# Kernel tuning notes

Measured on AMD Instinct MI355X. Metric: run time of the kernel, lower is better.

## Reference

```python
import jax, jax.numpy as jnp
import numpy as np

NEG_SLOPE = 0.2


def gat_conv(x, src, dst, W, a_src, a_dst, b, concat):
    # x: [N, Fin]; W: [H*C, Fin]; a_src/a_dst: [H, C]; b: [H*C] or [C]
    N = x.shape[0]
    H, C = a_src.shape
    h = (x @ W.T).reshape(N, H, C)                      # per-head transform
    s_n = jnp.sum(h * a_src, axis=-1)                   # [N, H]
    d_n = jnp.sum(h * a_dst, axis=-1)                   # [N, H]
    e = jax.nn.leaky_relu(s_n[src] + d_n[dst], NEG_SLOPE)  # [E, H]
    # segment softmax over incoming edges of each destination node
    m = jax.ops.segment_max(e, dst, num_segments=N)
    m = jnp.where(jnp.isfinite(m), m, 0.0)
    ex = jnp.exp(e - m[dst])
    denom = jax.ops.segment_sum(ex, dst, num_segments=N)
    alpha = ex / (denom[dst] + 1e-16)                    # [E, H]
    msg = h[src] * alpha[:, :, None]                     # [E, H, C]
    out = jax.ops.segment_sum(msg, dst, num_segments=N)  # [N, H, C]
    out = out.reshape(N, H * C) if concat else out.mean(axis=1)
    return out + b


def setup_inputs() -> dict:
    key = jax.random.key(0)
    ks = jax.random.split(key, 16)
    N, E, F, C, H = 50000, 800000, 256, 128, 4
    sc = lambda fan_in: 1.0 / np.sqrt(fan_in)
    inp = {
        "x": jax.random.normal(ks[0], (N, F), dtype=jnp.float32),
        "edge_index": jax.random.randint(ks[1], (2, E), 0, N, dtype=jnp.int64),
        # layer 1: F -> H*C (concat)
        "W1": jax.random.normal(ks[2], (H * C, F), jnp.float32) * sc(F),
        "a_src1": jax.random.normal(ks[3], (H, C), jnp.float32) * sc(C),
        "a_dst1": jax.random.normal(ks[4], (H, C), jnp.float32) * sc(C),
        "b1": jnp.zeros((H * C,), jnp.float32),
        # layer 2: H*C -> H*C (concat)
        "W2": jax.random.normal(ks[5], (H * C, H * C), jnp.float32) * sc(H * C),
        "a_src2": jax.random.normal(ks[6], (H, C), jnp.float32) * sc(C),
        "a_dst2": jax.random.normal(ks[7], (H, C), jnp.float32) * sc(C),
        "b2": jnp.zeros((H * C,), jnp.float32),
        # layer 3: H*C -> C (heads=1, concat=False)
        "W3": jax.random.normal(ks[8], (C, H * C), jnp.float32) * sc(H * C),
        "a_src3": jax.random.normal(ks[9], (1, C), jnp.float32) * sc(C),
        "a_dst3": jax.random.normal(ks[10], (1, C), jnp.float32) * sc(C),
        "b3": jnp.zeros((C,), jnp.float32),
        # allocation head: C -> C//2 -> 1
        "Wh1": jax.random.normal(ks[11], (C // 2, C), jnp.float32) * sc(C),
        "bh1": jnp.zeros((C // 2,), jnp.float32),
        "Wh2": jax.random.normal(ks[12], (1, C // 2), jnp.float32) * sc(C // 2),
        "bh2": jnp.zeros((1,), jnp.float32),
    }
    return inp


def reference(x, edge_index, W1, a_src1, a_dst1, b1, W2, a_src2, a_dst2, b2,
              W3, a_src3, a_dst3, b3, Wh1, bh1, Wh2, bh2):
    N = x.shape[0]
    loops = jnp.arange(N, dtype=edge_index.dtype)
    src = jnp.concatenate([edge_index[0], loops])  # self-loops (PyG default)
    dst = jnp.concatenate([edge_index[1], loops])

    h = gat_conv(x, src, dst, W1, a_src1, a_dst1, b1, concat=True)
    h = jax.nn.elu(h)  # dropout is identity at inference
    h = gat_conv(h, src, dst, W2, a_src2, a_dst2, b2, concat=True)
    h = jax.nn.elu(h)
    embeddings = gat_conv(h, src, dst, W3, a_src3, a_dst3, b3, concat=False)

    z = jax.nn.relu(embeddings @ Wh1.T + bh1)
    allocation_scores = jax.nn.sigmoid(z @ Wh2.T + bh2)
    return embeddings, allocation_scores
```

## Files before the change

kernel.cpp:

```cpp
#include <hip/hip_runtime.h>
#include <math.h>

typedef _Float16 f16;
typedef f16 f16x2 __attribute__((ext_vector_type(2)));
typedef f16 f16x8 __attribute__((ext_vector_type(8)));
typedef float f32x4 __attribute__((ext_vector_type(4)));

template <int V> struct VecT;
template <> struct VecT<2> { using T = f16 __attribute__((ext_vector_type(2))); };
template <> struct VecT<8> { using T = f16 __attribute__((ext_vector_type(8))); };

__device__ __forceinline__ unsigned ordf(float f) {
  unsigned u = __float_as_uint(f);
  return (u >> 31) ? ~u : (u | 0x80000000u);
}
__device__ __forceinline__ float unordf(unsigned u) {
  return (u >> 31) ? __uint_as_float(u & 0x7fffffffu) : __uint_as_float(~u);
}


__global__ void k_count(const int* __restrict__ dstArr, int* __restrict__ cnt,
                        int E, int Et) {
  int i = blockIdx.x * blockDim.x + threadIdx.x;
  if (i >= Et) return;
  int d = (i < E) ? dstArr[i] : (i - E);
  atomicAdd(&cnt[d], 1);
}

__global__ __launch_bounds__(256) void k_scanA(const int* __restrict__ cnt,
                                               int* __restrict__ row_ptr,
                                               int* __restrict__ bsum, int n) {
  __shared__ int part[256];
  int t = threadIdx.x;
  int base = blockIdx.x * 1024 + t * 4;
  int4 v = make_int4(0, 0, 0, 0);
  if (base + 3 < n) v = *(const int4*)&cnt[base];
  else {
    if (base + 0 < n) v.x = cnt[base + 0];
    if (base + 1 < n) v.y = cnt[base + 1];
    if (base + 2 < n) v.z = cnt[base + 2];
    if (base + 3 < n) v.w = cnt[base + 3];
  }
  int s = v.x + v.y + v.z + v.w;
  part[t] = s;
  __syncthreads();
  for (int off = 1; off < 256; off <<= 1) {
    int x = (t >= off) ? part[t - off] : 0;
    __syncthreads();
    part[t] += x;
    __syncthreads();
  }
  int p0 = (t == 0) ? 0 : part[t - 1];
  int p1 = p0 + v.x, p2 = p1 + v.y, p3 = p2 + v.z;
  if (base + 0 < n) row_ptr[base + 0] = p0;
  if (base + 1 < n) row_ptr[base + 1] = p1;
  if (base + 2 < n) row_ptr[base + 2] = p2;
  if (base + 3 < n) row_ptr[base + 3] = p3;
  if (t == 255) bsum[blockIdx.x] = part[255];
}

__global__ __launch_bounds__(1024) void k_scanB(int* __restrict__ bsum, int nb) {
  __shared__ int part[1024];
  int t = threadIdx.x;
  int v = (t < nb) ? bsum[t] : 0;
  part[t] = v;
  __syncthreads();
  for (int off = 1; off < 1024; off <<= 1) {
    int x = (t >= off) ? part[t - off] : 0;
    __syncthreads();
    part[t] += x;
    __syncthreads();
  }
  if (t < nb) bsum[t] = (t == 0) ? 0 : part[t - 1];
  if (t == 1023) bsum[nb] = part[1023];
}

__global__ void k_scanC(int* __restrict__ row_ptr, int* __restrict__ cursor,
                        const int* __restrict__ bsum, int n, int nb) {
  int i = blockIdx.x * blockDim.x + threadIdx.x;
  if (i < n) {
    int v = row_ptr[i] + bsum[i >> 10];
    row_ptr[i] = v;
    cursor[i] = v;
  }
  if (i == n) row_ptr[n] = bsum[nb];
}

__global__ void k_fill(const int* __restrict__ dstArr, int* __restrict__ cursor,
                       int* __restrict__ perm, int E, int Et) {
  int i = blockIdx.x * blockDim.x + threadIdx.x;
  if (i >= Et) return;
  int d = (i < E) ? dstArr[i] : (i - E);
  int pos = atomicAdd(&cursor[d], 1);
  perm[pos] = i;
}

__global__ void k_f2h4(const float* s0, f16* d0, int n0,
                       const float* s1, f16* d1, int n1,
                       const float* s2, f16* d2, int n2,
                       const float* s3, f16* d3, int n3) {
  int i = blockIdx.x * blockDim.x + threadIdx.x;
  const float* s; f16* d;
  if (i < n0) { s = s0; d = d0; }
  else if ((i -= n0) < n1) { s = s1; d = d1; }
  else if ((i -= n1) < n2) { s = s2; d = d2; }
  else if ((i -= n2) < n3) { s = s3; d = d3; }
  else return;
  float4 v = ((const float4*)s)[i];
  union { f16 h[4]; double dd; } u;
  u.h[0] = (f16)v.x; u.h[1] = (f16)v.y; u.h[2] = (f16)v.z; u.h[3] = (f16)v.w;
  ((double*)d)[i] = u.dd;
}

__global__ __launch_bounds__(256) void k_hgemm_nt(
    const f16* __restrict__ A, const f16* __restrict__ B,
    f16* __restrict__ C, int M, int Nn, int K,
    const float* __restrict__ a_src, const float* __restrict__ a_dst,
    float* __restrict__ sArr, float* __restrict__ dArr,
    unsigned* __restrict__ gmaxU, int H) {
  __shared__ f16 As[128 * 32];
  __shared__ f16 Bs[128 * 32];
  int tid = threadIdx.x;
  int wave = tid >> 6, lane = tid & 63;
  int quad = lane >> 4, l16 = lane & 15;
  int m0 = blockIdx.y * 128, n0 = blockIdx.x * 128;
  int wm = (wave & 1) * 64, wn = (wave >> 1) * 64;

  int lr = lane >> 2;
  int lc = lane & 3;
  int chunk = lc ^ ((lr >> 1) & 3);
  int rb0 = wave * 16;
  int rb1 = 64 + wave * 16;
  int ga0 = m0 + rb0 + lr; if (ga0 >= M) ga0 = M - 1;
  int ga1 = m0 + rb1 + lr; if (ga1 >= M) ga1 = M - 1;
  const f16* gA0 = A + (size_t)ga0 * K + chunk * 8;
  const f16* gA1 = A + (size_t)ga1 * K + chunk * 8;
  const f16* gB0 = B + (size_t)(n0 + rb0 + lr) * K + chunk * 8;
  const f16* gB1 = B + (size_t)(n0 + rb1 + lr) * K + chunk * 8;
  f16* lA0 = &As[rb0 * 32];
  f16* lA1 = &As[rb1 * 32];
  f16* lB0 = &Bs[rb0 * 32];
  f16* lB1 = &Bs[rb1 * 32];

  int rsw = (quad ^ ((l16 >> 1) & 3)) * 8;
  const f16* Ard[4];
  const f16* Brd[4];
#pragma unroll
  for (int i = 0; i < 4; ++i) {
    Ard[i] = &As[(wm + i * 16 + l16) * 32 + rsw];
    Brd[i] = &Bs[(wn + i * 16 + l16) * 32 + rsw];
  }

  f32x4 acc[4][4];
#pragma unroll
  for (int i = 0; i < 4; ++i)
#pragma unroll
    for (int j = 0; j < 4; ++j) acc[i][j] = (f32x4)(0.f);

  for (int k0 = 0; k0 < K; k0 += 32) {
    __syncthreads();
    __builtin_amdgcn_global_load_lds(
        (const __attribute__((address_space(1))) void*)(gA0 + k0),
        (__attribute__((address_space(3))) void*)lA0, 16, 0, 0);
    __builtin_amdgcn_global_load_lds(
        (const __attribute__((address_space(1))) void*)(gA1 + k0),
        (__attribute__((address_space(3))) void*)lA1, 16, 0, 0);
    __builtin_amdgcn_global_load_lds(
        (const __attribute__((address_space(1))) void*)(gB0 + k0),
        (__attribute__((address_space(3))) void*)lB0, 16, 0, 0);
    __builtin_amdgcn_global_load_lds(
        (const __attribute__((address_space(1))) void*)(gB1 + k0),
        (__attribute__((address_space(3))) void*)lB1, 16, 0, 0);
    __syncthreads();
    f16x8 af[4], bf[4];
#pragma unroll
    for (int i = 0; i < 4; ++i) af[i] = *(const f16x8*)Ard[i];
#pragma unroll
    for (int j = 0; j < 4; ++j) bf[j] = *(const f16x8*)Brd[j];
#pragma unroll
    for (int i = 0; i < 4; ++i)
#pragma unroll
      for (int j = 0; j < 4; ++j)
        acc[i][j] = __builtin_amdgcn_mfma_f32_16x16x32_f16(af[i], bf[j], acc[i][j], 0, 0, 0);
  }

#pragma unroll
  for (int i = 0; i < 4; ++i) {
#pragma unroll
    for (int r = 0; r < 4; ++r) {
      int m = m0 + wm + i * 16 + quad * 4 + r;
      if (m < M) {
        f16* Cp = C + (size_t)m * Nn + n0 + wn + l16;
#pragma unroll
        for (int j = 0; j < 4; ++j) Cp[j * 16] = (f16)acc[i][j][r];
      }
    }
  }

  float av[4], ad[4];
#pragma unroll
  for (int j = 0; j < 4; ++j) {
    int col = n0 + wn + l16 + j * 16;
    av[j] = a_src[col];
    ad[j] = a_dst[col];
  }
  float sp[16], dp[16];
#pragma unroll
  for (int i = 0; i < 4; ++i)
#pragma unroll
    for (int r = 0; r < 4; ++r) {
      float ss = 0.f, dd = 0.f;
#pragma unroll
      for (int j = 0; j < 4; ++j) {
        ss += acc[i][j][r] * av[j];
        dd += acc[i][j][r] * ad[j];
      }
#pragma unroll
      for (int msk = 1; msk < 16; msk <<= 1) {
        ss += __shfl_xor(ss, msk);
        dd += __shfl_xor(dd, msk);
      }
      sp[i * 4 + r] = ss;
      dp[i * 4 + r] = dd;
    }

  __syncthreads();
  float* fb = (float*)As;
  int wv = wn >> 6;
  if (l16 == 0) {
#pragma unroll
    for (int i = 0; i < 4; ++i)
#pragma unroll
      for (int r = 0; r < 4; ++r) {
        int row = wm + i * 16 + quad * 4 + r;
        fb[wv * 128 + row] = sp[i * 4 + r];
        fb[256 + wv * 128 + row] = dp[i * 4 + r];
      }
  }
  __syncthreads();
  if (tid < 128) {
    int m = m0 + tid;
    if (m < M) {
      float s = fb[tid] + fb[128 + tid];
      float d = fb[256 + tid] + fb[384 + tid];
      int head = n0 >> 7;
      sArr[(size_t)m * H + head] = s;
      dArr[(size_t)m * H + head] = d;
      atomicMax(&gmaxU[head], ordf(s));
    }
  }
}

template <int HH, int CT, bool DOELU, typename OutT>
__global__ __launch_bounds__(256) void k_aggregate(
    const f16* __restrict__ hin, const float* __restrict__ sArr,
    const float* __restrict__ dArr, const int* __restrict__ row_ptr,
    const int* __restrict__ perm, const int* __restrict__ srcArr,
    const unsigned* __restrict__ gmaxU, const float* __restrict__ bias,
    OutT* __restrict__ outp, int N, int E) {
  constexpr int VEC = CT / 64;
  constexpr int CPER = CT / HH;
  using gvec = typename VecT<VEC>::T;

  __shared__ int2 pairs[4][64 * HH];

  int wave = threadIdx.x >> 6;
  int lane = threadIdx.x & 63;
  int n = blockIdx.x * 4 + wave;
  if (n >= N) return;
  int e0 = row_ptr[n];
  int deg = row_ptr[n + 1] - e0;

  const int myhead = (HH == 1) ? 0 : (lane * VEC) / CPER;
  const int laneByte = lane * VEC * 2;

  float dloc[HH], mn[HH];
#pragma unroll
  for (int h = 0; h < HH; ++h) {
    dloc[h] = dArr[n * HH + h];
    float m = unordf(gmaxU[h]) + dloc[h];
    mn[h] = (m > 0.f) ? m : 0.2f * m;
  }

  float acc[VEC];
#pragma unroll
  for (int k = 0; k < VEC; ++k) acc[k] = 0.f;
  float dsum[HH];
#pragma unroll
  for (int h = 0; h < HH; ++h) dsum[h] = 0.f;

  int2* pw = &pairs[wave][0];

#define LOADG(VB, WB, g)                                                      \
  do {                                                                        \
    _Pragma("unroll") for (int j_ = 0; j_ < 4; ++j_) {                        \
      int2 p_ = pw[((g) * 4 + j_) * HH + myhead];                             \
      WB[j_] = __int_as_float(p_.y);                                          \
      VB[j_] = *(const gvec*)((const char*)hin + (unsigned)(p_.x + laneByte));\
    }                                                                         \
  } while (0)

#define FMAG(VB, WB)                                                          \
  do {                                                                        \
    _Pragma("unroll") for (int j_ = 0; j_ < 4; ++j_)                          \
        _Pragma("unroll") for (int k_ = 0; k_ < VEC; ++k_)                    \
            acc[k_] += WB[j_] * (float)VB[j_][k_];                            \
  } while (0)

  for (int base = 0; base < deg; base += 64) {
    int cn = min(64, deg - base);

    int soff = 0;
    float w_l[HH];
#pragma unroll
    for (int h = 0; h < HH; ++h) w_l[h] = 0.f;
    if (lane < cn) {
      int eid = perm[e0 + base + lane];
      int s = (eid < E) ? srcArr[eid] : (eid - E);
      soff = s * (CT * 2);
      if (HH == 4) {
        float4 sv = ((const float4*)sArr)[s];
        float svv[4] = {sv.x, sv.y, sv.z, sv.w};
#pragma unroll
        for (int h = 0; h < 4; ++h) {
          float e = svv[h] + dloc[h];
          e = (e > 0.f) ? e : 0.2f * e;
          w_l[h] = __expf(e - mn[h]);
        }
      } else {
        float e = sArr[s] + dloc[0];
        e = (e > 0.f) ? e : 0.2f * e;
        w_l[0] = __expf(e - mn[0]);
      }
    }
#pragma unroll
    for (int h = 0; h < HH; ++h) dsum[h] += w_l[h];

    if (HH == 4) {
      int4 p0 = make_int4(soff, __float_as_int(w_l[0]), soff, __float_as_int(w_l[1]));
      int4 p1 = make_int4(soff, __float_as_int(w_l[2]), soff, __float_as_int(w_l[3]));
      *(int4*)&pw[lane * 4] = p0;
      *(int4*)&pw[lane * 4 + 2] = p1;
    } else {
      pw[lane] = make_int2(soff, __float_as_int(w_l[0]));
    }
    asm volatile("s_waitcnt lgkmcnt(0)" ::: "memory");

    int cng = (cn + 3) >> 2;
    gvec vA[4], vB[4];
    float wA[4], wB[4];
    LOADG(vA, wA, 0);
    int g = 0;
    while (g + 2 < cng) {
      LOADG(vB, wB, g + 1);
      FMAG(vA, wA);
      LOADG(vA, wA, g + 2);
      FMAG(vB, wB);
      g += 2;
    }
    if (g + 1 < cng) {
      LOADG(vB, wB, g + 1);
      FMAG(vA, wA);
      FMAG(vB, wB);
    } else {
      FMAG(vA, wA);
    }
  }
#undef LOADG
#undef FMAG

  float dn;
  if (HH == 4) {
    float t0 = dsum[0], t1 = dsum[1], t2 = dsum[2], t3 = dsum[3];
#pragma unroll
    for (int m = 1; m < 64; m <<= 1) {
      t0 += __shfl_xor(t0, m);
      t1 += __shfl_xor(t1, m);
      t2 += __shfl_xor(t2, m);
      t3 += __shfl_xor(t3, m);
    }
    dn = (myhead < 2) ? (myhead == 0 ? t0 : t1) : (myhead == 2 ? t2 : t3);
  } else {
    float t0 = dsum[0];
#pragma unroll
    for (int m = 1; m < 64; m <<= 1) t0 += __shfl_xor(t0, m);
    dn = t0;
  }
  dn += 1e-16f;

  struct alignas(sizeof(OutT) * VEC) OutV { OutT v[VEC]; } ov;
#pragma unroll
  for (int k = 0; k < VEC; ++k) {
    float v = acc[k] / dn + bias[lane * VEC + k];
    if (DOELU) v = (v > 0.f) ? v : expm1f(v);
    ov.v[k] = (OutT)v;
  }
  *(OutV*)(outp + (size_t)n * CT + lane * VEC) = ov;
}

__global__ __launch_bounds__(256) void k_head(
    const float* __restrict__ emb, const float* __restrict__ Wh1,
    const float* __restrict__ bh1, const float* __restrict__ Wh2,
    const float* __restrict__ bh2, float* __restrict__ scores, int N) {
  __shared__ float w1s[64 * 132];
  __shared__ float w2s[64];
  __shared__ float b1s[64];
  int t = threadIdx.x;
  for (int i = t; i < 64 * 32; i += 256) {
    int r = i >> 5, c4 = i & 31;
    float4 v = ((const float4*)Wh1)[i];
    *(float4*)&w1s[r * 132 + c4 * 4] = v;
  }
  if (t < 64) { w2s[t] = Wh2[t]; b1s[t] = bh1[t]; }
  __syncthreads();
  float b2v = bh2[0];
  int wave = t >> 6, lane = t & 63;
  int gw = blockIdx.x * 4 + wave;
  int nw = gridDim.x * 4;
  for (int n = gw; n < N; n += nw) {
    float2 xv = ((const float2*)(emb + (size_t)n * 128))[lane];
    float z = b1s[lane];
#pragma unroll
    for (int j = 0; j < 32; ++j) {
      float4 w = *(const float4*)&w1s[lane * 132 + 4 * j];
      float a0 = __shfl(xv.x, 2 * j);
      float a1 = __shfl(xv.y, 2 * j);
      float a2 = __shfl(xv.x, 2 * j + 1);
      float a3 = __shfl(xv.y, 2 * j + 1);
      z += w.x * a0 + w.y * a1 + w.z * a2 + w.w * a3;
    }
    z = fmaxf(z, 0.f);
    float v = z * w2s[lane];
#pragma unroll
    for (int off = 32; off; off >>= 1) v += __shfl_down(v, off);
    if (lane == 0) scores[n] = 1.f / (1.f + __expf(-(v + b2v)));
  }
}


extern "C" void kernel_launch(void* const* d_in, const int* in_sizes, int n_in,
                              void* d_out, int out_size, void* d_ws, size_t ws_size,
                              hipStream_t stream) {
  const float* x   = (const float*)d_in[0];
  const int*   ei  = (const int*)d_in[1];
  const float* W1  = (const float*)d_in[2];
  const float* as1 = (const float*)d_in[3];
  const float* ad1 = (const float*)d_in[4];
  const float* b1  = (const float*)d_in[5];
  const float* W2  = (const float*)d_in[6];
  const float* as2 = (const float*)d_in[7];
  const float* ad2 = (const float*)d_in[8];
  const float* b2  = (const float*)d_in[9];
  const float* W3  = (const float*)d_in[10];
  const float* as3 = (const float*)d_in[11];
  const float* ad3 = (const float*)d_in[12];
  const float* b3  = (const float*)d_in[13];
  const float* Wh1 = (const float*)d_in[14];
  const float* bh1 = (const float*)d_in[15];
  const float* Wh2 = (const float*)d_in[16];
  const float* bh2 = (const float*)d_in[17];
  float* out = (float*)d_out;

  const int F = 256, HC = 512, H = 4, C = 128;
  const int N = in_sizes[0] / F;
  const int E = in_sizes[1] / 2;
  const int Et = E + N;
  const int* srcArr = ei;
  const int* dstArr = ei + E;

  char* ws = (char*)d_ws;
  size_t off = 0;
  auto alloc = [&](size_t bytes) -> void* {
    void* p = ws + off;
    off += (bytes + 255) & ~(size_t)255;
    return p;
  };
  f16*   h16    = (f16*)alloc((size_t)N * HC * 2);
  f16*   hAgg   = (f16*)alloc((size_t)N * HC * 2);
  f16*   xh     = (f16*)alloc((size_t)N * F * 2);
  f16*   W1h    = (f16*)alloc((size_t)HC * F * 2);
  f16*   W2h    = (f16*)alloc((size_t)HC * HC * 2);
  f16*   W3h    = (f16*)alloc((size_t)C * HC * 2);
  int* row_ptr  = (int*)alloc((size_t)(N + 1) * 4);
  char* zr      = (char*)alloc((size_t)N * 4 + 64);
  int* cnt      = (int*)zr;
  unsigned* gm1 = (unsigned*)(zr + (size_t)N * 4);
  unsigned* gm2 = gm1 + 4;
  unsigned* gm3 = gm1 + 8;
  int* cursor   = (int*)alloc((size_t)N * 4);
  int* perm     = (int*)alloc((size_t)Et * 4);
  float* sArr   = (float*)alloc((size_t)N * H * 4);
  float* dArr   = (float*)alloc((size_t)N * H * 4);
  int* bsum     = (int*)alloc((size_t)1028 * 4);
  (void)ws_size; (void)n_in; (void)out_size;

  hipMemsetAsync(zr, 0, (size_t)N * 4 + 64, stream);
  int eb = (Et + 255) / 256;
  int nb = (N + 1023) / 1024;
  k_count<<<eb, 256, 0, stream>>>(dstArr, cnt, E, Et);
  k_scanA<<<nb, 256, 0, stream>>>(cnt, row_ptr, bsum, N);
  k_scanB<<<1, 1024, 0, stream>>>(bsum, nb);
  k_scanC<<<(N + 256) / 256, 256, 0, stream>>>(row_ptr, cursor, bsum, N, nb);
  k_fill<<<eb, 256, 0, stream>>>(dstArr, cursor, perm, E, Et);

  int c0 = N * F / 4, c1 = HC * F / 4, c2 = HC * HC / 4, c3 = C * HC / 4;
  int ctot = c0 + c1 + c2 + c3;
  k_f2h4<<<(ctot + 255) / 256, 256, 0, stream>>>(x, xh, c0, W1, W1h, c1,
                                                 W2, W2h, c2, W3, W3h, c3);

  int aggGrid = (N + 3) / 4;
  dim3 g1(HC / 128, (N + 127) / 128);
  dim3 g3(C / 128, (N + 127) / 128);

  k_hgemm_nt<<<g1, 256, 0, stream>>>(xh, W1h, h16, N, HC, F,
                                     as1, ad1, sArr, dArr, gm1, H);
  k_aggregate<4, 512, true, f16><<<aggGrid, 256, 0, stream>>>(
      h16, sArr, dArr, row_ptr, perm, srcArr, gm1, b1, hAgg, N, E);

  k_hgemm_nt<<<g1, 256, 0, stream>>>(hAgg, W2h, h16, N, HC, HC,
                                     as2, ad2, sArr, dArr, gm2, H);
  k_aggregate<4, 512, true, f16><<<aggGrid, 256, 0, stream>>>(
      h16, sArr, dArr, row_ptr, perm, srcArr, gm2, b2, hAgg, N, E);

  k_hgemm_nt<<<g3, 256, 0, stream>>>(hAgg, W3h, h16, N, C, HC,
                                     as3, ad3, sArr, dArr, gm3, 1);
  k_aggregate<1, 128, false, float><<<aggGrid, 256, 0, stream>>>(
      h16, sArr, dArr, row_ptr, perm, srcArr, gm3, b3, out, N, E);

  k_head<<<512, 256, 0, stream>>>(out, Wh1, bh1, Wh2, bh2, out + (size_t)N * C, N);
}
```

Before: 846.4 us.

## Double-buffer GEMM LDS, swizzle blocks across XCDs, store source ids directly in CSR

The GEMM now double-buffers its LDS tiles, issuing the next K-slice's global-to-LDS loads before computing on the current one, which hides load latency behind MFMA work. It also switches to a 1D grid remapped so consecutive tiles land on the same XCD, aiming for better L2 reuse of the A rows. The CSR fill stores source node ids directly instead of edge permutation indices, removing a dependent gather in every aggregate pass. The aggregate kernel's LDS pair buffer is re-laid out head-major so each lane reads contiguously. The cost is twice the GEMM LDS footprint and hand-written waitcnt/barrier sequencing.

```diff
diff --git a/kernel.cpp b/kernel.cpp
--- a/kernel.cpp
+++ b/kernel.cpp
@@ -86,13 +86,16 @@
   if (i == n) row_ptr[n] = bsum[nb];
 }
 
-__global__ void k_fill(const int* __restrict__ dstArr, int* __restrict__ cursor,
-                       int* __restrict__ perm, int E, int Et) {
+__global__ void k_fill(const int* __restrict__ dstArr,
+                       const int* __restrict__ srcArr, int* __restrict__ cursor,
+                       int* __restrict__ esrc, int E, int Et) {
   int i = blockIdx.x * blockDim.x + threadIdx.x;
   if (i >= Et) return;
-  int d = (i < E) ? dstArr[i] : (i - E);
+  int d, s;
+  if (i < E) { d = dstArr[i]; s = srcArr[i]; }
+  else       { d = i - E; s = d; }
   int pos = atomicAdd(&cursor[d], 1);
-  perm[pos] = i;
+  esrc[pos] = s;
 }
 
 __global__ void k_f2h4(const float* s0, f16* d0, int n0,
@@ -114,16 +117,25 @@
 
 __global__ __launch_bounds__(256) void k_hgemm_nt(
     const f16* __restrict__ A, const f16* __restrict__ B,
-    f16* __restrict__ C, int M, int Nn, int K,
+    f16* __restrict__ C, int M, int Nn, int K, int nbx,
     const float* __restrict__ a_src, const float* __restrict__ a_dst,
     float* __restrict__ sArr, float* __restrict__ dArr,
     unsigned* __restrict__ gmaxU, int H) {
-  __shared__ f16 As[128 * 32];
-  __shared__ f16 Bs[128 * 32];
+  __shared__ f16 As[2 * 128 * 32];
+  __shared__ f16 Bs[2 * 128 * 32];
   int tid = threadIdx.x;
   int wave = tid >> 6, lane = tid & 63;
   int quad = lane >> 4, l16 = lane & 15;
-  int m0 = blockIdx.y * 128, n0 = blockIdx.x * 128;
+
+  int nwg = gridDim.x;
+  int orig = blockIdx.x;
+  int q = nwg >> 3, r = nwg & 7;
+  int xcd = orig & 7, pos = orig >> 3;
+  int swz = (xcd < r) ? (xcd * (q + 1) + pos)
+                      : (r * (q + 1) + (xcd - r) * q + pos);
+  int bx = swz % nbx;
+  int by = swz / nbx;
+  int m0 = by * 128, n0 = bx * 128;
   int wm = (wave & 1) * 64, wn = (wave >> 1) * 64;
 
   int lr = lane >> 2;
@@ -137,10 +149,6 @@
   const f16* gA1 = A + (size_t)ga1 * K + chunk * 8;
   const f16* gB0 = B + (size_t)(n0 + rb0 + lr) * K + chunk * 8;
   const f16* gB1 = B + (size_t)(n0 + rb1 + lr) * K + chunk * 8;
-  f16* lA0 = &As[rb0 * 32];
-  f16* lA1 = &As[rb1 * 32];
-  f16* lB0 = &Bs[rb0 * 32];
-  f16* lB1 = &Bs[rb1 * 32];
 
   int rsw = (quad ^ ((l16 >> 1) & 3)) * 8;
   const f16* Ard[4];
@@ -157,32 +165,42 @@
 #pragma unroll
     for (int j = 0; j < 4; ++j) acc[i][j] = (f32x4)(0.f);
 
-  for (int k0 = 0; k0 < K; k0 += 32) {
-    __syncthreads();
-    __builtin_amdgcn_global_load_lds(
-        (const __attribute__((address_space(1))) void*)(gA0 + k0),
-        (__attribute__((address_space(3))) void*)lA0, 16, 0, 0);
-    __builtin_amdgcn_global_load_lds(
-        (const __attribute__((address_space(1))) void*)(gA1 + k0),
-        (__attribute__((address_space(3))) void*)lA1, 16, 0, 0);
-    __builtin_amdgcn_global_load_lds(
-        (const __attribute__((address_space(1))) void*)(gB0 + k0),
-        (__attribute__((address_space(3))) void*)lB0, 16, 0, 0);
-    __builtin_amdgcn_global_load_lds(
-        (const __attribute__((address_space(1))) void*)(gB1 + k0),
-        (__attribute__((address_space(3))) void*)lB1, 16, 0, 0);
-    __syncthreads();
+#define GLDS(gp, lp)                                                     \
+  __builtin_amdgcn_global_load_lds(                                      \
+      (const __attribute__((address_space(1))) void*)(gp),               \
+      (__attribute__((address_space(3))) void*)(lp), 16, 0, 0)
+#define STAGE(buf, kk)                                                   \
+  do {                                                                   \
+    GLDS(gA0 + (kk), As + (buf) * 4096 + rb0 * 32);                      \
+    GLDS(gA1 + (kk), As + (buf) * 4096 + rb1 * 32);                      \
+    GLDS(gB0 + (kk), Bs + (buf) * 4096 + rb0 * 32);                      \
+    GLDS(gB1 + (kk), Bs + (buf) * 4096 + rb1 * 32);                      \
+  } while (0)
+
+  int nt = K >> 5;
+  STAGE(0, 0);
+  for (int t = 0; t < nt; ++t) {
+    int cur = t & 1;
+    if (t + 1 < nt) {
+      STAGE(cur ^ 1, (t + 1) << 5);
+      asm volatile("s_waitcnt vmcnt(4)\n\ts_barrier" ::: "memory");
+    } else {
+      asm volatile("s_waitcnt vmcnt(0)\n\ts_barrier" ::: "memory");
+    }
     f16x8 af[4], bf[4];
 #pragma unroll
-    for (int i = 0; i < 4; ++i) af[i] = *(const f16x8*)Ard[i];
-#pragma unroll
-    for (int j = 0; j < 4; ++j) bf[j] = *(const f16x8*)Brd[j];
+    for (int i = 0; i < 4; ++i) af[i] = *(const f16x8*)(Ard[i] + cur * 4096);
+#pragma unroll
+    for (int j = 0; j < 4; ++j) bf[j] = *(const f16x8*)(Brd[j] + cur * 4096);
 #pragma unroll
     for (int i = 0; i < 4; ++i)
 #pragma unroll
       for (int j = 0; j < 4; ++j)
         acc[i][j] = __builtin_amdgcn_mfma_f32_16x16x32_f16(af[i], bf[j], acc[i][j], 0, 0, 0);
-  }
+    asm volatile("s_barrier" ::: "memory");
+  }
+#undef STAGE
+#undef GLDS
 
 #pragma unroll
   for (int i = 0; i < 4; ++i) {
@@ -255,14 +273,13 @@
 __global__ __launch_bounds__(256) void k_aggregate(
     const f16* __restrict__ hin, const float* __restrict__ sArr,
     const float* __restrict__ dArr, const int* __restrict__ row_ptr,
-    const int* __restrict__ perm, const int* __restrict__ srcArr,
-    const unsigned* __restrict__ gmaxU, const float* __restrict__ bias,
-    OutT* __restrict__ outp, int N, int E) {
+    const int* __restrict__ esrc, const unsigned* __restrict__ gmaxU,
+    const float* __restrict__ bias, OutT* __restrict__ outp, int N, int E) {
   constexpr int VEC = CT / 64;
   constexpr int CPER = CT / HH;
   using gvec = typename VecT<VEC>::T;
 
-  __shared__ int2 pairs[4][64 * HH];
+  __shared__ int2 pairs[4][HH * 64];
 
   int wave = threadIdx.x >> 6;
   int lane = threadIdx.x & 63;
@@ -290,11 +307,12 @@
   for (int h = 0; h < HH; ++h) dsum[h] = 0.f;
 
   int2* pw = &pairs[wave][0];
+  const int2* pr = &pairs[wave][myhead * 64];
 
 #define LOADG(VB, WB, g)                                                      \
   do {                                                                        \
     _Pragma("unroll") for (int j_ = 0; j_ < 4; ++j_) {                        \
-      int2 p_ = pw[((g) * 4 + j_) * HH + myhead];                             \
+      int2 p_ = pr[(g) * 4 + j_];                                             \
       WB[j_] = __int_as_float(p_.y);                                          \
       VB[j_] = *(const gvec*)((const char*)hin + (unsigned)(p_.x + laneByte));\
     }                                                                         \
@@ -315,8 +333,7 @@
 #pragma unroll
     for (int h = 0; h < HH; ++h) w_l[h] = 0.f;
     if (lane < cn) {
-      int eid = perm[e0 + base + lane];
-      int s = (eid < E) ? srcArr[eid] : (eid - E);
+      int s = esrc[e0 + base + lane];
       soff = s * (CT * 2);
       if (HH == 4) {
         float4 sv = ((const float4*)sArr)[s];
@@ -336,14 +353,9 @@
 #pragma unroll
     for (int h = 0; h < HH; ++h) dsum[h] += w_l[h];
 
-    if (HH == 4) {
-      int4 p0 = make_int4(soff, __float_as_int(w_l[0]), soff, __float_as_int(w_l[1]));
-      int4 p1 = make_int4(soff, __float_as_int(w_l[2]), soff, __float_as_int(w_l[3]));
-      *(int4*)&pw[lane * 4] = p0;
-      *(int4*)&pw[lane * 4 + 2] = p1;
-    } else {
-      pw[lane] = make_int2(soff, __float_as_int(w_l[0]));
-    }
+#pragma unroll
+    for (int h = 0; h < HH; ++h)
+      pw[h * 64 + lane] = make_int2(soff, __float_as_int(w_l[h]));
     asm volatile("s_waitcnt lgkmcnt(0)" ::: "memory");
 
     int cng = (cn + 3) >> 2;
@@ -488,7 +500,7 @@
   unsigned* gm2 = gm1 + 4;
   unsigned* gm3 = gm1 + 8;
   int* cursor   = (int*)alloc((size_t)N * 4);
-  int* perm     = (int*)alloc((size_t)Et * 4);
+  int* esrc     = (int*)alloc((size_t)Et * 4);
   float* sArr   = (float*)alloc((size_t)N * H * 4);
   float* dArr   = (float*)alloc((size_t)N * H * 4);
   int* bsum     = (int*)alloc((size_t)1028 * 4);
@@ -501,7 +513,7 @@
   k_scanA<<<nb, 256, 0, stream>>>(cnt, row_ptr, bsum, N);
   k_scanB<<<1, 1024, 0, stream>>>(bsum, nb);
   k_scanC<<<(N + 256) / 256, 256, 0, stream>>>(row_ptr, cursor, bsum, N, nb);
-  k_fill<<<eb, 256, 0, stream>>>(dstArr, cursor, perm, E, Et);
+  k_fill<<<eb, 256, 0, stream>>>(dstArr, srcArr, cursor, esrc, E, Et);
 
   int c0 = N * F / 4, c1 = HC * F / 4, c2 = HC * HC / 4, c3 = C * HC / 4;
   int ctot = c0 + c1 + c2 + c3;
@@ -509,23 +521,24 @@
                                                  W2, W2h, c2, W3, W3h, c3);
 
   int aggGrid = (N + 3) / 4;
-  dim3 g1(HC / 128, (N + 127) / 128);
-  dim3 g3(C / 128, (N + 127) / 128);
-
-  k_hgemm_nt<<<g1, 256, 0, stream>>>(xh, W1h, h16, N, HC, F,
-                                     as1, ad1, sArr, dArr, gm1, H);
+  int mblk = (N + 127) / 128;
+  int nblk1 = 4 * mblk;
+  int nblk3 = mblk;
+
+  k_hgemm_nt<<<nblk1, 256, 0, stream>>>(xh, W1h, h16, N, HC, F, 4,
+                                        as1, ad1, sArr, dArr, gm1, H);
   k_aggregate<4, 512, true, f16><<<aggGrid, 256, 0, stream>>>(
-      h16, sArr, dArr, row_ptr, perm, srcArr, gm1, b1, hAgg, N, E);
-
-  k_hgemm_nt<<<g1, 256, 0, stream>>>(hAgg, W2h, h16, N, HC, HC,
-                                     as2, ad2, sArr, dArr, gm2, H);
+      h16, sArr, dArr, row_ptr, esrc, gm1, b1, hAgg, N, E);
+
+  k_hgemm_nt<<<nblk1, 256, 0, stream>>>(hAgg, W2h, h16, N, HC, HC, 4,
+                                        as2, ad2, sArr, dArr, gm2, H);
   k_aggregate<4, 512, true, f16><<<aggGrid, 256, 0, stream>>>(
-      h16, sArr, dArr, row_ptr, perm, srcArr, gm2, b2, hAgg, N, E);
-
-  k_hgemm_nt<<<g3, 256, 0, stream>>>(hAgg, W3h, h16, N, C, HC,
-                                     as3, ad3, sArr, dArr, gm3, 1);
+      h16, sArr, dArr, row_ptr, esrc, gm2, b2, hAgg, N, E);
+
+  k_hgemm_nt<<<nblk3, 256, 0, stream>>>(hAgg, W3h, h16, N, C, HC, 1,
+                                        as3, ad3, sArr, dArr, gm3, 1);
   k_aggregate<1, 128, false, float><<<aggGrid, 256, 0, stream>>>(
-      h16, sArr, dArr, row_ptr, perm, srcArr, gm3, b3, out, N, E);
+      h16, sArr, dArr, row_ptr, esrc, gm3, b3, out, N, E);
 
   k_head<<<512, 256, 0, stream>>>(out, Wh1, bh1, Wh2, bh2, out + (size_t)N * C, N);
 }
```

After: 788.6 us. 1.07x faster.
